# Kernel tuning notes

Measured on AMD Instinct MI355X. Metric: run time of the kernel, lower is better.

The kernel has to match this reference:

```python
import jax, jax.numpy as jnp
import numpy as np
from jax import lax

B, C, H, W = 16, 128, 128, 128
K = 3
EPS = 1e-8


def setup_inputs() -> dict:
    key = jax.random.key(0)
    k1, k2, k3 = jax.random.split(key, 3)
    x = jax.random.normal(k1, (B, C, H, W), dtype=jnp.float32)
    style = jax.random.normal(k2, (B, C), dtype=jnp.float32)
    weight = jax.random.normal(k3, (C, C, K, K), dtype=jnp.float32)
    return {"x": x, "style": style, "weight": weight}


def reference(x, style, weight):
    b = x.shape[0]
    o, i, kh, kw = weight.shape
    h, w_sp = x.shape[2], x.shape[3]
    # style / ||style||_inf over channel dim (per-sample scalar)
    s = style / jnp.max(jnp.abs(style), axis=1, keepdims=True)          # (B, i)
    # weight * (1/sqrt(i*kh*kw)) / ||weight||_inf over (i,kh,kw) per out channel
    wmax = jnp.max(jnp.abs(weight), axis=(1, 2, 3), keepdims=True)      # (o,1,1,1)
    wn = weight * (1.0 / jnp.sqrt(jnp.float32(i * kh * kw)) / wmax)     # (o,i,kh,kw)
    # per-sample modulation over input channels
    wmod = wn[None] * s[:, None, :, None, None]                         # (B,o,i,kh,kw)
    # demodulation (coe reshaped to (i,1,1,1) in torch; valid since o==i)
    coe = lax.rsqrt(jnp.sum(jnp.square(wmod), axis=(2, 3, 4)) + EPS)    # (B,o)
    wmod = wmod * coe[:, :, None, None, None]
    # fused batched conv via grouped-conv trick (StyleGAN2-style)
    xr = x.reshape(1, b * i, h, w_sp)
    wr = wmod.reshape(b * o, i, kh, kw)
    out = lax.conv_general_dilated(
        xr, wr,
        window_strides=(1, 1),
        padding=[(1, 1), (1, 1)],
        feature_group_count=b,
        dimension_numbers=("NCHW", "OIHW", "NCHW"),
    )
    return out.reshape(b, o, h, w_sp)
```

## Files before the change

kernel.cpp:

```cpp
#include <hip/hip_runtime.h>
#include <hip/hip_bf16.h>


#define BATCH 16
#define CH    128
#define HW    128
#define WPITCH 1152

#define WS_WMAX 0
#define WS_SN   128
#define WS_AFAC 2176
#define WS_WT   4224
#define WFRAG_BYTE_OFF 606720
#define WFRAG_BYTES    4718592
#define WS_NEEDED      (WFRAG_BYTE_OFF + WFRAG_BYTES)

typedef short  s8v  __attribute__((ext_vector_type(8)));
typedef float  f4v  __attribute__((ext_vector_type(4)));

__device__ inline unsigned short f2bf(float f) {
    union { float f; unsigned int u; } v; v.f = f;
    unsigned int r = v.u + 0x7FFFu + ((v.u >> 16) & 1u);
    return (unsigned short)(r >> 16);
}

__global__ __launch_bounds__(256) void k0_transpose(const float* __restrict__ w,
                                                    float* __restrict__ ws) {
    int idx = blockIdx.x * 256 + threadIdx.x;
    if (idx < CH * WPITCH) {
        int kt = idx >> 7;
        int o  = idx & 127;
        ws[WS_WT + idx] = w[(size_t)o * WPITCH + kt];
    }
}

__global__ __launch_bounds__(256) void k1_norms(const float* __restrict__ style,
                                                const float* __restrict__ weight,
                                                float* __restrict__ ws) {
    __shared__ float red[4];
    const int bid = blockIdx.x;
    const int t = threadIdx.x;
    if (bid < 128) {
        const int o = bid;
        float m = 0.f;
        for (int idx = t; idx < WPITCH; idx += 256)
            m = fmaxf(m, fabsf(weight[(size_t)o * WPITCH + idx]));
        #pragma unroll
        for (int off = 32; off > 0; off >>= 1)
            m = fmaxf(m, __shfl_down(m, off, 64));
        if ((t & 63) == 0) red[t >> 6] = m;
        __syncthreads();
        if (t == 0)
            ws[WS_WMAX + o] = fmaxf(fmaxf(red[0], red[1]), fmaxf(red[2], red[3]));
    } else {
        const int b = bid - 128;
        float v = (t < CH) ? style[b * CH + t] : 0.f;
        float m = fabsf(v);
        #pragma unroll
        for (int off = 32; off > 0; off >>= 1)
            m = fmaxf(m, __shfl_down(m, off, 64));
        if ((t & 63) == 0) red[t >> 6] = m;
        __syncthreads();
        float smax = fmaxf(fmaxf(red[0], red[1]), fmaxf(red[2], red[3]));
        if (t < CH) ws[WS_SN + b * CH + t] = v / smax;
    }
}

__global__ __launch_bounds__(256) void k2_coe(const float* __restrict__ weight,
                                              float* __restrict__ ws) {
    const int o = blockIdx.x;
    const int b = blockIdx.y;
    const int t = threadIdx.x;
    const float* sn = ws + WS_SN + b * CH;
    float s = 0.f;
    for (int idx = t; idx < WPITCH; idx += 256) {
        int i = idx / 9;
        float v = weight[(size_t)o * WPITCH + idx] * sn[i];
        s += v * v;
    }
    #pragma unroll
    for (int off = 32; off > 0; off >>= 1) s += __shfl_down(s, off, 64);
    __shared__ float red[4];
    if ((t & 63) == 0) red[t >> 6] = s;
    __syncthreads();
    if (t == 0) {
        float S = red[0] + red[1] + red[2] + red[3];
        float wm = ws[WS_WMAX + o];
        float scale = 1.0f / (sqrtf(1152.0f) * wm);
        float coe = rsqrtf(scale * scale * S + 1e-8f);
        ws[WS_AFAC + b * CH + o] = scale * coe;
    }
}

__global__ __launch_bounds__(256) void k3_swz(const float* __restrict__ ws,
                                              unsigned short* __restrict__ wfrag) {
    int t = blockIdx.x * 256 + threadIdx.x;
    const int lane = t & 63;
    int f = t >> 6;
    const int mo = f & 7;  f >>= 3;
    const int ci = f & 3;  f >>= 2;
    const int kk = f % 9;
    const int b  = f / 9;
    const int o  = mo * 16 + (lane & 15);
    const int i0 = ci * 32 + (lane >> 4) * 8;
    const float af = ws[WS_AFAC + b * CH + o];
    union { unsigned short u[8]; uint4 v; } pk;
    #pragma unroll
    for (int j = 0; j < 8; ++j) {
        int i = i0 + j;
        float v = ws[WS_WT + (size_t)(i * 9 + kk) * 128 + o] * af * ws[WS_SN + b * CH + i];
        pk.u[j] = f2bf(v);
    }
    *(uint4*)(wfrag + (size_t)t * 8) = pk.v;
}

#define XROW 132
#define XIP  40

__global__ __launch_bounds__(256, 2) void k4_mfma(const float* __restrict__ x,
                                                  const unsigned short* __restrict__ wfrag,
                                                  float* __restrict__ out) {
    const int h0 = blockIdx.x * 2;
    const int b  = blockIdx.y;
    const int t  = threadIdx.x;
    const int lane = t & 63;
    const int w    = t >> 6;
    const int ohalf = w & 1;
    const int rsel  = w >> 1;
    const int ln15  = lane & 15;
    const int quad  = lane >> 4;

    __shared__ unsigned short xT[4 * XROW * XIP];

    f4v acc[4][8];
    #pragma unroll
    for (int mt = 0; mt < 4; ++mt)
        #pragma unroll
        for (int nt = 0; nt < 8; ++nt)
            acc[mt][nt] = (f4v){0.f, 0.f, 0.f, 0.f};

    #pragma unroll 1
    for (int ci = 0; ci < 4; ++ci) {
        const int ib = ci * 32;
        __syncthreads();

        #pragma unroll 1
        for (int idx = t; idx < 16 * 130; idx += 256) {
            int c  = idx % 130;
            int ri = idx / 130;
            int r   = ri & 3;
            int ibk = ri >> 2;
            int row = h0 - 1 + r;
            int col = c - 1;
            union { unsigned short u[8]; s8v v; } pk;
            if ((unsigned)row < 128u && (unsigned)col < 128u) {
                const float* xp = x + (((size_t)(b * CH + ib + ibk * 8)) * HW + row) * HW + col;
                #pragma unroll
                for (int j = 0; j < 8; ++j)
                    pk.u[j] = f2bf(xp[(size_t)j * HW * HW]);
            } else {
                #pragma unroll
                for (int j = 0; j < 8; ++j) pk.u[j] = 0;
            }
            *(s8v*)&xT[(r * XROW + c) * XIP + ibk * 8] = pk.v;
        }
        __syncthreads();

        #pragma unroll 1
        for (int ky = 0; ky < 3; ++ky) {
            const int r = rsel + ky;
            #pragma unroll 1
            for (int kx = 0; kx < 3; ++kx) {
                const int kk = ky * 3 + kx;
                s8v a[4];
                #pragma unroll
                for (int mt = 0; mt < 4; ++mt) {
                    int mo = ohalf * 4 + mt;
                    size_t off = ((size_t)(((b * 9 + kk) * 4 + ci) * 8 + mo) * 64 + lane) * 8;
                    a[mt] = *(const s8v*)(wfrag + off);
                }
                s8v bf[8];
                #pragma unroll
                for (int nt = 0; nt < 8; ++nt) {
                    int c = nt * 16 + ln15 + kx;
                    bf[nt] = *(const s8v*)&xT[(r * XROW + c) * XIP + quad * 8];
                }
                #pragma unroll
                for (int mt = 0; mt < 4; ++mt)
                    #pragma unroll
                    for (int nt = 0; nt < 8; ++nt)
                        acc[mt][nt] = __builtin_amdgcn_mfma_f32_16x16x32_bf16(
                            a[mt], bf[nt], acc[mt][nt], 0, 0, 0);
            }
        }
    }

    const int orow = h0 + rsel;
    #pragma unroll
    for (int mt = 0; mt < 4; ++mt) {
        int o = ohalf * 64 + mt * 16 + quad * 4;
        #pragma unroll
        for (int nt = 0; nt < 8; ++nt) {
            int xcol = nt * 16 + ln15;
            float* op = out + (((size_t)(b * CH + o)) * HW + orow) * HW + xcol;
            #pragma unroll
            for (int reg = 0; reg < 4; ++reg)
                op[(size_t)reg * HW * HW] = acc[mt][nt][reg];
        }
    }
}

#define TI    8
#define XPITCH 132
__global__ __launch_bounds__(256) void k3_conv(const float* __restrict__ x,
                                               const float* __restrict__ ws,
                                               float* __restrict__ out) {
    const int h = blockIdx.x;
    const int b = blockIdx.y;
    const int t = threadIdx.x;
    const int og = t >> 4;
    const int pg = t & 15;

    __shared__ float x_lds[TI * 3 * XPITCH];
    __shared__ float w_lds[TI * 9 * 128];
    __shared__ float Af_l[128];
    __shared__ float sn_l[128];

    if (t < 128) {
        Af_l[t] = ws[WS_AFAC + b * CH + t];
        sn_l[t] = ws[WS_SN + b * CH + t];
    }
    float acc[8][8];
    #pragma unroll
    for (int j = 0; j < 8; ++j)
        #pragma unroll
        for (int p = 0; p < 8; ++p) acc[j][p] = 0.f;

    const float4* wt4 = (const float4*)(ws + WS_WT);
    float4* w_lds4 = (float4*)w_lds;
    const float4* Af4 = (const float4*)Af_l;

    #pragma unroll 1
    for (int ci = 0; ci < CH / TI; ++ci) {
        const int ib = ci * TI;
        __syncthreads();
        for (int idx = t; idx < TI * 3 * 130; idx += 256) {
            int ti  = idx / 390;
            int rem = idx - ti * 390;
            int r   = rem / 130;
            int c   = rem - r * 130;
            int row = h + r - 1;
            int col = c - 1;
            float v = 0.f;
            if ((unsigned)row < 128u && (unsigned)col < 128u)
                v = x[(((size_t)b * CH + ib + ti) * HW + row) * HW + col];
            x_lds[(ti * 3 + r) * XPITCH + c] = v;
        }
        for (int idx = t; idx < TI * 9 * 32; idx += 256) {
            int kt = idx >> 5;
            int o4 = idx & 31;
            int ti = kt / 9;
            float4 wv = wt4[(size_t)ib * 9 * 32 + idx];
            float4 af = Af4[o4];
            float  s  = sn_l[ib + ti];
            float4 rr;
            rr.x = wv.x * af.x * s; rr.y = wv.y * af.y * s;
            rr.z = wv.z * af.z * s; rr.w = wv.w * af.w * s;
            w_lds4[idx] = rr;
        }
        __syncthreads();
        #pragma unroll 1
        for (int ti = 0; ti < TI; ++ti) {
            float xv[3][12];
            #pragma unroll
            for (int ky = 0; ky < 3; ++ky)
                #pragma unroll
                for (int q = 0; q < 3; ++q) {
                    float4 v = *(const float4*)&x_lds[(ti * 3 + ky) * XPITCH + pg * 8 + q * 4];
                    xv[ky][q*4+0] = v.x; xv[ky][q*4+1] = v.y;
                    xv[ky][q*4+2] = v.z; xv[ky][q*4+3] = v.w;
                }
            #pragma unroll
            for (int kk = 0; kk < 9; ++kk) {
                const int ky = kk / 3;
                const int kx = kk % 3;
                float wv[8];
                #pragma unroll
                for (int q = 0; q < 2; ++q) {
                    float4 v = *(const float4*)&w_lds[(ti * 9 + kk) * 128 + og * 8 + q * 4];
                    wv[q*4+0] = v.x; wv[q*4+1] = v.y; wv[q*4+2] = v.z; wv[q*4+3] = v.w;
                }
                #pragma unroll
                for (int j = 0; j < 8; ++j)
                    #pragma unroll
                    for (int p = 0; p < 8; ++p)
                        acc[j][p] = fmaf(wv[j], xv[ky][p + kx], acc[j][p]);
            }
        }
    }
    const size_t obase = ((size_t)b * CH) * (HW * HW) + (size_t)h * HW;
    #pragma unroll
    for (int j = 0; j < 8; ++j) {
        int o = og * 8 + j;
        float4 v0 = {acc[j][0], acc[j][1], acc[j][2], acc[j][3]};
        float4 v1 = {acc[j][4], acc[j][5], acc[j][6], acc[j][7]};
        *(float4*)&out[obase + (size_t)o * (HW * HW) + pg * 8]     = v0;
        *(float4*)&out[obase + (size_t)o * (HW * HW) + pg * 8 + 4] = v1;
    }
}

extern "C" void kernel_launch(void* const* d_in, const int* in_sizes, int n_in,
                              void* d_out, int out_size, void* d_ws, size_t ws_size,
                              hipStream_t stream) {
    const float* x      = (const float*)d_in[0];
    const float* style  = (const float*)d_in[1];
    const float* weight = (const float*)d_in[2];
    float* out = (float*)d_out;
    float* ws  = (float*)d_ws;

    k0_transpose<<<(CH * WPITCH + 255) / 256, 256, 0, stream>>>(weight, ws);
    k1_norms<<<144, 256, 0, stream>>>(style, weight, ws);
    k2_coe<<<dim3(CH, BATCH), 256, 0, stream>>>(weight, ws);

    if (ws_size >= (size_t)WS_NEEDED) {
        unsigned short* wfrag = (unsigned short*)((char*)d_ws + WFRAG_BYTE_OFF);
        k3_swz<<<1152, 256, 0, stream>>>(ws, wfrag);
        k4_mfma<<<dim3(HW / 2, BATCH), 256, 0, stream>>>(x, wfrag, out);
    } else {
        k3_conv<<<dim3(HW, BATCH), 256, 0, stream>>>(x, ws, out);
    }
}
```

Before: 315.0 us.

## Factor style modulation into input and demod into output, share bf16 weights across batch

The per-sample weight modulation is moved out of the weight fragments. Style scaling is now applied to x while it is staged into LDS, and the demodulation coefficient is applied to the accumulators at store time, so one batch-independent bf16 weight fragment set is built (16x smaller, and the swizzle grid shrinks to match). The LDS x tile also drops its padding in favour of an XOR slot swizzle against bank conflicts, and launch bounds are raised to 4 blocks per SM. This cuts weight-fragment global traffic and the prep kernel, at the cost of extra multiplies during x staging and a different bf16 rounding point.

```diff
diff --git a/kernel.cpp b/kernel.cpp
--- a/kernel.cpp
+++ b/kernel.cpp
@@ -9,10 +9,10 @@
 
 #define WS_WMAX 0
 #define WS_SN   128
-#define WS_AFAC 2176
+#define WS_COE  2176
 #define WS_WT   4224
 #define WFRAG_BYTE_OFF 606720
-#define WFRAG_BYTES    4718592
+#define WFRAG_BYTES    294912
 #define WS_NEEDED      (WFRAG_BYTE_OFF + WFRAG_BYTES)
 
 typedef short  s8v  __attribute__((ext_vector_type(8)));
@@ -87,8 +87,7 @@
         float S = red[0] + red[1] + red[2] + red[3];
         float wm = ws[WS_WMAX + o];
         float scale = 1.0f / (sqrtf(1152.0f) * wm);
-        float coe = rsqrtf(scale * scale * S + 1e-8f);
-        ws[WS_AFAC + b * CH + o] = scale * coe;
+        ws[WS_COE + b * CH + o] = rsqrtf(scale * scale * S + 1e-8f);
     }
 }
 
@@ -97,28 +96,27 @@
     int t = blockIdx.x * 256 + threadIdx.x;
     const int lane = t & 63;
     int f = t >> 6;
-    const int mo = f & 7;  f >>= 3;
-    const int ci = f & 3;  f >>= 2;
-    const int kk = f % 9;
-    const int b  = f / 9;
+    const int mo = f & 7;
+    const int ci = (f >> 3) & 3;
+    const int kk = f >> 5;
     const int o  = mo * 16 + (lane & 15);
     const int i0 = ci * 32 + (lane >> 4) * 8;
-    const float af = ws[WS_AFAC + b * CH + o];
+    const float scale = 1.0f / (sqrtf(1152.0f) * ws[WS_WMAX + o]);
     union { unsigned short u[8]; uint4 v; } pk;
     #pragma unroll
     for (int j = 0; j < 8; ++j) {
         int i = i0 + j;
-        float v = ws[WS_WT + (size_t)(i * 9 + kk) * 128 + o] * af * ws[WS_SN + b * CH + i];
-        pk.u[j] = f2bf(v);
+        pk.u[j] = f2bf(ws[WS_WT + (size_t)(i * 9 + kk) * 128 + o] * scale);
     }
     *(uint4*)(wfrag + (size_t)t * 8) = pk.v;
 }
 
-#define XROW 132
-#define XIP  40
-
-__global__ __launch_bounds__(256, 2) void k4_mfma(const float* __restrict__ x,
+#define XROW 130
+#define XIP  32
+
+__global__ __launch_bounds__(256, 4) void k4_mfma(const float* __restrict__ x,
                                                   const unsigned short* __restrict__ wfrag,
+                                                  const float* __restrict__ ws,
                                                   float* __restrict__ out) {
     const int h0 = blockIdx.x * 2;
     const int b  = blockIdx.y;
@@ -131,6 +129,13 @@
     const int quad  = lane >> 4;
 
     __shared__ unsigned short xT[4 * XROW * XIP];
+    __shared__ float sn_l[128];
+    __shared__ float coe_l[128];
+
+    if (t < 128) {
+        sn_l[t]  = ws[WS_SN + b * CH + t];
+        coe_l[t] = ws[WS_COE + b * CH + t];
+    }
 
     f4v acc[4][8];
     #pragma unroll
@@ -157,12 +162,13 @@
                 const float* xp = x + (((size_t)(b * CH + ib + ibk * 8)) * HW + row) * HW + col;
                 #pragma unroll
                 for (int j = 0; j < 8; ++j)
-                    pk.u[j] = f2bf(xp[(size_t)j * HW * HW]);
+                    pk.u[j] = f2bf(xp[(size_t)j * HW * HW] * sn_l[ib + ibk * 8 + j]);
             } else {
                 #pragma unroll
                 for (int j = 0; j < 8; ++j) pk.u[j] = 0;
             }
-            *(s8v*)&xT[(r * XROW + c) * XIP + ibk * 8] = pk.v;
+            int slot = ibk ^ ((c >> 1) & 3);
+            *(s8v*)&xT[(r * XROW + c) * XIP + slot * 8] = pk.v;
         }
         __syncthreads();
 
@@ -176,14 +182,15 @@
                 #pragma unroll
                 for (int mt = 0; mt < 4; ++mt) {
                     int mo = ohalf * 4 + mt;
-                    size_t off = ((size_t)(((b * 9 + kk) * 4 + ci) * 8 + mo) * 64 + lane) * 8;
+                    size_t off = ((size_t)((kk * 4 + ci) * 8 + mo) * 64 + lane) * 8;
                     a[mt] = *(const s8v*)(wfrag + off);
                 }
                 s8v bf[8];
                 #pragma unroll
                 for (int nt = 0; nt < 8; ++nt) {
                     int c = nt * 16 + ln15 + kx;
-                    bf[nt] = *(const s8v*)&xT[(r * XROW + c) * XIP + quad * 8];
+                    int slot = quad ^ ((c >> 1) & 3);
+                    bf[nt] = *(const s8v*)&xT[(r * XROW + c) * XIP + slot * 8];
                 }
                 #pragma unroll
                 for (int mt = 0; mt < 4; ++mt)
@@ -199,13 +206,14 @@
     #pragma unroll
     for (int mt = 0; mt < 4; ++mt) {
         int o = ohalf * 64 + mt * 16 + quad * 4;
+        float4 coe4 = *(const float4*)&coe_l[o];
         #pragma unroll
         for (int nt = 0; nt < 8; ++nt) {
             int xcol = nt * 16 + ln15;
             float* op = out + (((size_t)(b * CH + o)) * HW + orow) * HW + xcol;
             #pragma unroll
             for (int reg = 0; reg < 4; ++reg)
-                op[(size_t)reg * HW * HW] = acc[mt][nt][reg];
+                op[(size_t)reg * HW * HW] = acc[mt][nt][reg] * (&coe4.x)[reg];
         }
     }
 }
@@ -223,12 +231,12 @@
 
     __shared__ float x_lds[TI * 3 * XPITCH];
     __shared__ float w_lds[TI * 9 * 128];
-    __shared__ float Af_l[128];
-    __shared__ float sn_l[128];
+    __shared__ float coe_f[128];
+    __shared__ float sn_f[128];
 
     if (t < 128) {
-        Af_l[t] = ws[WS_AFAC + b * CH + t];
-        sn_l[t] = ws[WS_SN + b * CH + t];
+        coe_f[t] = ws[WS_COE + b * CH + t] / (sqrtf(1152.0f) * ws[WS_WMAX + t]);
+        sn_f[t]  = ws[WS_SN + b * CH + t];
     }
     float acc[8][8];
     #pragma unroll
@@ -238,7 +246,7 @@
 
     const float4* wt4 = (const float4*)(ws + WS_WT);
     float4* w_lds4 = (float4*)w_lds;
-    const float4* Af4 = (const float4*)Af_l;
+    const float4* Af4 = (const float4*)coe_f;
 
     #pragma unroll 1
     for (int ci = 0; ci < CH / TI; ++ci) {
@@ -262,7 +270,7 @@
             int ti = kt / 9;
             float4 wv = wt4[(size_t)ib * 9 * 32 + idx];
             float4 af = Af4[o4];
-            float  s  = sn_l[ib + ti];
+            float  s  = sn_f[ib + ti];
             float4 rr;
             rr.x = wv.x * af.x * s; rr.y = wv.y * af.y * s;
             rr.z = wv.z * af.z * s; rr.w = wv.w * af.w * s;
@@ -324,8 +332,8 @@
 
     if (ws_size >= (size_t)WS_NEEDED) {
         unsigned short* wfrag = (unsigned short*)((char*)d_ws + WFRAG_BYTE_OFF);
-        k3_swz<<<1152, 256, 0, stream>>>(ws, wfrag);
-        k4_mfma<<<dim3(HW / 2, BATCH), 256, 0, stream>>>(x, wfrag, out);
+        k3_swz<<<72, 256, 0, stream>>>(ws, wfrag);
+        k4_mfma<<<dim3(HW / 2, BATCH), 256, 0, stream>>>(x, wfrag, ws, out);
     } else {
         k3_conv<<<dim3(HW, BATCH), 256, 0, stream>>>(x, ws, out);
     }
```

New measurement: 1.001 ms. 218% more time.
